# Optimization experiments

Measured on AMD Instinct MI355X. Metric: run time of the kernel, lower is better.

## Reference

```python
import jax, jax.numpy as jnp
import numpy as np

N_NODES = 50000
N_EDGES = 1_600_000
HIDDEN = 128
BOND = 16


def setup_inputs() -> dict:
    key = jax.random.key(0)
    ks = jax.random.split(key, 6)
    h = jax.random.normal(ks[0], (N_NODES, HIDDEN), dtype=jnp.float32)
    edge_index = jax.random.randint(ks[1], (2, N_EDGES), 0, N_NODES, dtype=jnp.int32)
    bond_features = jax.random.normal(ks[2], (N_EDGES, BOND), dtype=jnp.float32)
    fan_in1 = 2 * HIDDEN + BOND
    W1 = jax.random.normal(ks[3], (fan_in1, HIDDEN), dtype=jnp.float32) / np.sqrt(fan_in1)
    b1 = jnp.zeros((HIDDEN,), dtype=jnp.float32)
    W2 = jax.random.normal(ks[4], (HIDDEN, HIDDEN), dtype=jnp.float32) / np.sqrt(HIDDEN)
    b2 = jnp.zeros((HIDDEN,), dtype=jnp.float32)
    return {"h": h, "edge_index": edge_index, "bond_features": bond_features,
            "W1": W1, "b1": b1, "W2": W2, "b2": b2}


def reference(h, edge_index, bond_features, W1, b1, W2, b2):
    row, col = edge_index[0], edge_index[1]
    # gather endpoint features + bond features -> [E, 2H+B]
    msgs = jnp.concatenate([h[row], h[col], bond_features], axis=-1)
    # 2-layer MLP with SiLU
    msgs = jax.nn.silu(msgs @ W1 + b1) @ W2 + b2  # [E, H]
    # scatter-add back to source nodes (index_add_ on row)
    h_out = jax.ops.segment_sum(msgs, row, num_segments=h.shape[0])
    return h_out
```

## Files before the change

kernel.cpp:

```cpp
#include <hip/hip_runtime.h>

typedef __attribute__((ext_vector_type(4))) float  f32x4;
typedef __attribute__((ext_vector_type(2))) float  f32x2;
typedef __attribute__((ext_vector_type(8))) short  s16x8;
typedef __attribute__((ext_vector_type(4))) float  f4v;
typedef __attribute__((ext_vector_type(4))) int    i32x4;

#define MFMA_BF16 __builtin_amdgcn_mfma_f32_16x16x32_bf16
#define SENT 0x7fffffff

#if defined(__has_builtin)
#if __has_builtin(__builtin_amdgcn_cvt_pk_fp8_f32) && __has_builtin(__builtin_amdgcn_cvt_pk_f32_fp8)
#define HW8 1
#endif
#endif

__device__ __forceinline__ short f2bf(float f) {
  unsigned u = __builtin_bit_cast(unsigned, f);
  u += 0x7fffu + ((u >> 16) & 1u);
  return (short)(u >> 16);
}
__device__ __forceinline__ float bf2f(short s) {
  unsigned u = ((unsigned)(unsigned short)s) << 16;
  return __builtin_bit_cast(float, u);
}
__device__ __forceinline__ s16x8 cvt8(f4v f0, f4v f1) {
  s16x8 r;
  r[0] = f2bf(f0[0]); r[1] = f2bf(f0[1]); r[2] = f2bf(f0[2]); r[3] = f2bf(f0[3]);
  r[4] = f2bf(f1[0]); r[5] = f2bf(f1[1]); r[6] = f2bf(f1[2]); r[7] = f2bf(f1[3]);
  return r;
}
__device__ __forceinline__ unsigned cvtpk_bf16(float a, float b) {
  unsigned r;
  asm("v_cvt_pk_bf16_f32 %0, %1, %2" : "=v"(r) : "v"(a), "v"(b));
  return r;
}
__device__ __forceinline__ unsigned f2fp8(float x) {
  unsigned u = __builtin_bit_cast(unsigned, x);
  unsigned s = (u >> 24) & 0x80u;
  unsigned au = u & 0x7fffffffu;
  if (au < 0x3C800000u) return s;
  unsigned biased = au - 0x3C000000u;
  unsigned val = biased >> 20;
  unsigned rem = biased & 0xFFFFFu;
  val += (rem > 0x80000u) || (rem == 0x80000u && (val & 1u));
  if (val > 0x7Eu) val = 0x7Eu;
  return s | val;
}
__device__ __forceinline__ float fp8tof(unsigned b) {
  unsigned em = b & 0x7fu;
  unsigned f = ((em + 960u) << 20) | ((b & 0x80u) << 24);
  return (em < 8u) ? 0.f : __builtin_bit_cast(float, f);
}
__device__ __forceinline__ unsigned char enc_fp8(float x) {
#ifdef HW8
  return (unsigned char)(__builtin_amdgcn_cvt_pk_fp8_f32(x, x, 0u, false) & 0xffu);
#else
  return (unsigned char)f2fp8(x);
#endif
}
__device__ __forceinline__ unsigned enc_fp8x4(f4v v) {
#ifdef HW8
  unsigned u = __builtin_amdgcn_cvt_pk_fp8_f32(v[0], v[1], 0u, false);
  u = __builtin_amdgcn_cvt_pk_fp8_f32(v[2], v[3], u, true);
  return u;
#else
  return f2fp8(v[0]) | (f2fp8(v[1]) << 8) | (f2fp8(v[2]) << 16) | (f2fp8(v[3]) << 24);
#endif
}
__device__ __forceinline__ void dec_fp8x4(unsigned d, float* f) {
#ifdef HW8
  f32x2 lo = __builtin_amdgcn_cvt_pk_f32_fp8(d, false);
  f32x2 hi = __builtin_amdgcn_cvt_pk_f32_fp8(d, true);
  f[0] = lo[0]; f[1] = lo[1]; f[2] = hi[0]; f[3] = hi[1];
#else
#pragma unroll
  for (int j = 0; j < 4; ++j) f[j] = fp8tof((d >> (8 * j)) & 0xffu);
#endif
}

__global__ __launch_bounds__(256) void prep_weights(
    const float* __restrict__ W1, const float* __restrict__ W2,
    short* __restrict__ wp, float* __restrict__ out, int outN4,
    int* __restrict__ cnt, int NN) {
  int t = blockIdx.x * 256 + threadIdx.x;
  int total = gridDim.x * 256;
  if (out) {
    f32x4* o4 = reinterpret_cast<f32x4*>(out);
    for (int i = t; i < outN4; i += total) o4[i] = (f32x4){0.f, 0.f, 0.f, 0.f};
  }
  if (cnt) {
    for (int i = t; i < NN; i += total) cnt[i] = 0;
  }
  int chunk = t >> 6, l = t & 63;
  if (chunk >= 104) return;
  int q = l >> 4, c = l & 15;
  s16x8 v;
  if (chunk < 72) {
    int kk = chunk >> 3, nt = chunk & 7;
    int k0 = kk * 32 + q * 8, n = nt * 16 + c;
#pragma unroll
    for (int j = 0; j < 8; ++j) {
      int k = k0 + j;
      v[j] = (k < 272) ? f2bf(W1[k * 128 + n]) : (short)0;
    }
    *reinterpret_cast<s16x8*>(wp + (size_t)chunk * 512 + l * 8) = v;
  } else {
    int c2 = chunk - 72;
    int kk = c2 >> 3, nt = c2 & 7;
    int k0 = kk * 32 + q * 8, n = nt * 16 + c;
#pragma unroll
    for (int j = 0; j < 8; ++j) v[j] = f2bf(W2[(k0 + j) * 128 + n]);
    *reinterpret_cast<s16x8*>(wp + 36864 + (size_t)c2 * 512 + l * 8) = v;
  }
}

#define NB_H 512
__global__ __launch_bounds__(256) void k_gh(
    const float* __restrict__ h, const short* __restrict__ wp,
    short* __restrict__ Gs, const int* __restrict__ ei,
    int* __restrict__ cnt, int NN, int NB_G, int E) {
  if ((int)blockIdx.x >= NB_G) {
    int i = ((int)blockIdx.x - NB_G) * 256 + threadIdx.x;
    for (; i < E; i += NB_H * 256) atomicAdd(&cnt[ei[i]], 1);
    return;
  }
  const int tid = threadIdx.x;
  const int w = tid >> 6, l = tid & 63;
  const int q = l >> 4, c = l & 15;
  const int nb = blockIdx.x * 64 + w * 16;

  f32x4 acc[16];
#pragma unroll
  for (int nt = 0; nt < 16; ++nt) acc[nt] = (f32x4){0.f, 0.f, 0.f, 0.f};

#pragma unroll
  for (int kk = 0; kk < 4; ++kk) {
    int node = nb + c; if (node >= NN) node = NN - 1;
    const float* src = h + (size_t)node * 128 + kk * 32 + q * 8;
    s16x8 a = cvt8(*reinterpret_cast<const f4v*>(src),
                   *reinterpret_cast<const f4v*>(src + 4));
#pragma unroll
    for (int nt2 = 0; nt2 < 16; ++nt2) {
      int kkg = kk + ((nt2 >= 8) ? 4 : 0);
      int chunk = kkg * 8 + (nt2 & 7);
      s16x8 b = *reinterpret_cast<const s16x8*>(wp + (size_t)chunk * 512 + l * 8);
      acc[nt2] = MFMA_BF16(a, b, acc[nt2], 0, 0, 0);
    }
  }
  unsigned char* Gb = (unsigned char*)Gs;
#pragma unroll
  for (int nt2 = 0; nt2 < 16; ++nt2)
#pragma unroll
    for (int r = 0; r < 4; ++r) {
      int node = nb + q * 4 + r;
      if (node < NN) {
        if (nt2 < 8) {
          Gs[(size_t)node * 192 + nt2 * 16 + c] = f2bf(acc[nt2][r]);
        } else {
          int n7 = nt2 - 8;
          int addr = ((n7 & 1) * 2 + (c >> 3)) * 32 + (n7 >> 1) * 8 + (c & 7);
          Gb[(size_t)node * 384 + 256 + addr] = enc_fp8(acc[nt2][r]);
        }
      }
    }
}

__global__ __launch_bounds__(1024) void k_s1(const int* __restrict__ cnt,
                                             int* __restrict__ partial, int NN) {
  __shared__ int red[16];
  int t = threadIdx.x, idx = blockIdx.x * 1024 + t;
  int v = (idx < NN) ? cnt[idx] : 0;
#pragma unroll
  for (int d = 1; d < 64; d <<= 1) v += __shfl_xor(v, d);
  if ((t & 63) == 0) red[t >> 6] = v;
  __syncthreads();
  if (t == 0) {
    int s = 0;
#pragma unroll
    for (int i = 0; i < 16; ++i) s += red[i];
    partial[blockIdx.x] = s;
  }
}
__global__ __launch_bounds__(1024) void k_s3m(int* __restrict__ cnt,
                                              const int* __restrict__ partial,
                                              int NN) {
  __shared__ int ps[1024];
  __shared__ int pbuf[64];
  __shared__ int base_s;
  int t = threadIdx.x, bid = blockIdx.x, idx = bid * 1024 + t;
  if (t < 64) pbuf[t] = (t < bid) ? partial[t] : 0;
  int v = (idx < NN) ? cnt[idx] : 0;
  ps[t] = v;
  __syncthreads();
  if (t == 0) {
    int b = 0;
#pragma unroll
    for (int j = 0; j < 64; ++j) b += pbuf[j];
    base_s = b;
  }
  for (int d = 1; d < 1024; d <<= 1) {
    int u = (t >= d) ? ps[t - d] : 0;
    __syncthreads(); ps[t] += u; __syncthreads();
  }
  if (idx < NN) cnt[idx] = ps[t] - v + base_s;
}

__global__ void k_scatter13(const int* __restrict__ ei, int* __restrict__ cnt,
                            int* __restrict__ rc, unsigned* __restrict__ bond8,
                            const float* __restrict__ bond, int E) {
  int i = blockIdx.x * blockDim.x + threadIdx.x;
  int stride = gridDim.x * blockDim.x;
  for (; i < E; i += stride) {
    int r = ei[i], c = ei[(size_t)E + i];
    int pos = atomicAdd(&cnt[r], 1);
    rc[pos] = r | (c << 16);
    const f4v* b4 = reinterpret_cast<const f4v*>(bond + (size_t)i * 16);
    i32x4 o;
    o[0] = (int)enc_fp8x4(b4[0]);
    o[1] = (int)enc_fp8x4(b4[1]);
    o[2] = (int)enc_fp8x4(b4[2]);
    o[3] = (int)enc_fp8x4(b4[3]);
    *reinterpret_cast<i32x4*>(bond8 + (size_t)pos * 4) = o;
  }
}

__global__ __launch_bounds__(512, 4) void edge_mlp14(
    const short* __restrict__ Gs, const int* __restrict__ rc,
    const unsigned* __restrict__ bond8, const short* __restrict__ wp,
    const float* __restrict__ b1, const float* __restrict__ b2,
    float* __restrict__ out, int E) {
  __shared__ __align__(16) char ubuf[8 * 16 * 136 * 2];
  __shared__ __align__(16) short wlds[20480];
  short (*Plds)[16][136] = reinterpret_cast<short(*)[16][136]>(ubuf);
  float (*Sred)[16][68]  = reinterpret_cast<float(*)[16][68]>(ubuf);

  const int tid = threadIdx.x;
  const int w = tid >> 6, l = tid & 63;
  const int q = l >> 4, c = l & 15;

  {
    const s16x8* src = reinterpret_cast<const s16x8*>(wp + 32768);
    s16x8* dst = reinterpret_cast<s16x8*>(wlds);
#pragma unroll
    for (int i = 0; i < 5; ++i) dst[tid + i * 512] = src[tid + i * 512];
  }
  __syncthreads();
  const short* wl1 = wlds;
  const short* wl2 = wlds + 4096;

  int nwg = gridDim.x;
  int qq = nwg >> 3, rr = nwg & 7;
  int xcd = blockIdx.x & 7, idx = blockIdx.x >> 3;
  int sbid = (xcd < rr ? xcd * (qq + 1) : rr * (qq + 1) + (xcd - rr) * qq) + idx;
  const int eb = sbid * 128;
  const int we = w * 16;

  int rcv = 0xFFFF;
  if (l < 16) {
    int gpos = eb + we + l;
    if (gpos < E) rcv = rc[gpos];
  }
  int v = __shfl(rcv, c);
  int rv = v & 0xffff;
  int rA = (rv == 0xFFFF) ? 0 : rv;
  int cA = ((unsigned)v) >> 16;

  int vn = __shfl(rcv, (l + 1) & 63);
  unsigned long long bm = __ballot(
      (l < 16) && ((rcv & 0xffff) != ((l < 15) ? (vn & 0xffff) : -1)));

  s16x8 g1v[4];
  i32x4 g2v[2];
  s16x8 az = {};
  {
    const short* gb = Gs + (size_t)rA * 192;
#pragma unroll
    for (int kk = 0; kk < 4; ++kk)
      g1v[kk] = *reinterpret_cast<const s16x8*>(gb + kk * 32 + q * 8);
    const char* g2b = (const char*)Gs + (size_t)cA * 384 + 256 + q * 32;
    g2v[0] = *reinterpret_cast<const i32x4*>(g2b);
    g2v[1] = *reinterpret_cast<const i32x4*>(g2b + 16);
    if (q < 2) {
      int ge = eb + we + c; if (ge >= E) ge = E - 1;
      uint2 d = *reinterpret_cast<const uint2*>(bond8 + (size_t)ge * 4 + q * 2);
      float f[8];
      dec_fp8x4(d.x, f);
      dec_fp8x4(d.y, f + 4);
      i32x4 aw;
#pragma unroll
      for (int p = 0; p < 4; ++p)
        aw[p] = (int)cvtpk_bf16(f[2 * p], f[2 * p + 1]);
      az = __builtin_bit_cast(s16x8, aw);
    }
  }

  f32x4 acc[8];
#pragma unroll
  for (int nt = 0; nt < 8; ++nt) acc[nt] = (f32x4){0.f, 0.f, 0.f, 0.f};
  __builtin_amdgcn_s_setprio(1);
#pragma unroll
  for (int nt = 0; nt < 8; ++nt) {
    s16x8 b = *reinterpret_cast<const s16x8*>(wl1 + nt * 512 + l * 8);
    acc[nt] = MFMA_BF16(az, b, acc[nt], 0, 0, 0);
  }
  __builtin_amdgcn_s_setprio(0);

#pragma unroll
  for (int nt = 0; nt < 8; ++nt) {
    float bias = b1[nt * 16 + c];
    unsigned p01 = cvtpk_bf16(acc[nt][0] + bias, acc[nt][1] + bias);
    unsigned p23 = cvtpk_bf16(acc[nt][2] + bias, acc[nt][3] + bias);
    Plds[w][q * 4 + 0][nt * 16 + c] = (short)(p01 & 0xffffu);
    Plds[w][q * 4 + 1][nt * 16 + c] = (short)(p01 >> 16);
    Plds[w][q * 4 + 2][nt * 16 + c] = (short)(p23 & 0xffffu);
    Plds[w][q * 4 + 3][nt * 16 + c] = (short)(p23 >> 16);
  }

#pragma unroll
  for (int nt = 0; nt < 8; ++nt) acc[nt] = (f32x4){0.f, 0.f, 0.f, 0.f};

#pragma unroll
  for (int kk = 0; kk < 4; ++kk) {
    s16x8 gk = g1v[kk];
    unsigned d0 = (unsigned)g2v[kk >> 1][(kk & 1) * 2 + 0];
    unsigned d1 = (unsigned)g2v[kk >> 1][(kk & 1) * 2 + 1];
    float g2f[8];
    dec_fp8x4(d0, g2f);
    dec_fp8x4(d1, g2f + 4);
    s16x8 pb = *reinterpret_cast<const s16x8*>(&Plds[w][c][kk * 32 + q * 8]);
    float sv[8];
#pragma unroll
    for (int j = 0; j < 8; ++j) {
      float x = bf2f(gk[j]) + g2f[j] + bf2f(pb[j]);
      float e = __expf(-x);
      sv[j] = x * __builtin_amdgcn_rcpf(1.f + e);
    }
    i32x4 a2w;
#pragma unroll
    for (int p = 0; p < 4; ++p)
      a2w[p] = (int)cvtpk_bf16(sv[2 * p], sv[2 * p + 1]);
    s16x8 a2 = __builtin_bit_cast(s16x8, a2w);
    __builtin_amdgcn_s_setprio(1);
#pragma unroll
    for (int nt = 0; nt < 8; ++nt) {
      s16x8 b = *reinterpret_cast<const s16x8*>(wl2 + (kk * 8 + nt) * 512 + l * 8);
      acc[nt] = MFMA_BF16(a2, b, acc[nt], 0, 0, 0);
    }
    __builtin_amdgcn_s_setprio(0);
  }

#pragma unroll
  for (int h2 = 0; h2 < 2; ++h2) {
#pragma unroll
    for (int nt2 = 0; nt2 < 4; ++nt2) {
      int nt = h2 * 4 + nt2;
      float bias = b2[nt * 16 + c];
#pragma unroll
      for (int r = 0; r < 4; ++r)
        Sred[w][q * 4 + r][nt2 * 16 + c] = acc[nt][r] + bias;
    }
    float vsum = 0.f;
#pragma unroll
    for (int r = 0; r < 16; ++r) {
      vsum += Sred[w][r][l];
      if ((bm >> r) & 1ull) {
        int rowv = __shfl(rcv, r) & 0xffff;
        if (rowv != 0xFFFF)
          unsafeAtomicAdd(&out[(size_t)rowv * 128 + h2 * 64 + l], vsum);
        vsum = 0.f;
      }
    }
  }
}

__global__ __launch_bounds__(256, 2) void edge_mlp(
    const float* __restrict__ h, const int* __restrict__ ei,
    const float* __restrict__ bond, const short* __restrict__ wp,
    const float* __restrict__ b1, const float* __restrict__ b2,
    float* __restrict__ out, int E) {
  __shared__ __align__(16) short Plds[4][64][136];
  __shared__ int rows_s[256];
  __shared__ int cols_s[256];
  const int tid = threadIdx.x;
  const int w = tid >> 6, l = tid & 63;
  const int q = l >> 4, c = l & 15;
  const int eb = blockIdx.x * 256;
  {
    int e = eb + tid; if (e >= E) e = E - 1;
    rows_s[tid] = ei[e];
    cols_s[tid] = ei[(size_t)E + e];
  }
  __syncthreads();
  const int we = w * 64;
  int rN[4], cN[4], eI[4];
#pragma unroll
  for (int mi = 0; mi < 4; ++mi) {
    int el = we + mi * 16 + c;
    rN[mi] = rows_s[el]; cN[mi] = cols_s[el];
    int eg = eb + el; if (eg >= E) eg = E - 1;
    eI[mi] = eg;
  }
  f32x4 acc[4][8];
#pragma unroll
  for (int mi = 0; mi < 4; ++mi)
#pragma unroll
    for (int nt = 0; nt < 8; ++nt) acc[mi][nt] = (f32x4){0.f, 0.f, 0.f, 0.f};
#pragma unroll
  for (int part = 0; part < 2; ++part) {
#pragma unroll
    for (int kk = 0; kk < 4; ++kk) {
      s16x8 a[4];
#pragma unroll
      for (int mi = 0; mi < 4; ++mi) {
        int node = part ? cN[mi] : rN[mi];
        const float* src = h + (size_t)node * 128 + kk * 32 + q * 8;
        a[mi] = cvt8(*reinterpret_cast<const f4v*>(src),
                     *reinterpret_cast<const f4v*>(src + 4));
      }
      const int kkg = part * 4 + kk;
#pragma unroll
      for (int nt = 0; nt < 8; ++nt) {
        s16x8 b = *reinterpret_cast<const s16x8*>(wp + (size_t)(kkg * 8 + nt) * 512 + l * 8);
#pragma unroll
        for (int mi = 0; mi < 4; ++mi)
          acc[mi][nt] = MFMA_BF16(a[mi], b, acc[mi][nt], 0, 0, 0);
      }
    }
  }
  {
    s16x8 a[4];
#pragma unroll
    for (int mi = 0; mi < 4; ++mi) {
      s16x8 az = {};
      if (q < 2) {
        const float* src = bond + (size_t)eI[mi] * 16 + q * 8;
        az = cvt8(*reinterpret_cast<const f4v*>(src),
                  *reinterpret_cast<const f4v*>(src + 4));
      }
      a[mi] = az;
    }
#pragma unroll
    for (int nt = 0; nt < 8; ++nt) {
      s16x8 b = *reinterpret_cast<const s16x8*>(wp + (size_t)(64 + nt) * 512 + l * 8);
#pragma unroll
      for (int mi = 0; mi < 4; ++mi)
        acc[mi][nt] = MFMA_BF16(a[mi], b, acc[mi][nt], 0, 0, 0);
    }
  }
#pragma unroll
  for (int nt = 0; nt < 8; ++nt) {
    float bias = b1[nt * 16 + c];
#pragma unroll
    for (int mi = 0; mi < 4; ++mi)
#pragma unroll
      for (int r = 0; r < 4; ++r) {
        float x = acc[mi][nt][r] + bias;
        float s = x / (1.f + __expf(-x));
        Plds[w][mi * 16 + q * 4 + r][nt * 16 + c] = f2bf(s);
      }
  }
  f32x4 acc2[4][8];
#pragma unroll
  for (int mi = 0; mi < 4; ++mi)
#pragma unroll
    for (int nt = 0; nt < 8; ++nt) acc2[mi][nt] = (f32x4){0.f, 0.f, 0.f, 0.f};
#pragma unroll
  for (int kk = 0; kk < 4; ++kk) {
    s16x8 a2[4];
#pragma unroll
    for (int mi = 0; mi < 4; ++mi)
      a2[mi] = *reinterpret_cast<const s16x8*>(&Plds[w][mi * 16 + c][kk * 32 + q * 8]);
#pragma unroll
    for (int nt = 0; nt < 8; ++nt) {
      s16x8 b = *reinterpret_cast<const s16x8*>(wp + 36864 + (size_t)(kk * 8 + nt) * 512 + l * 8);
#pragma unroll
      for (int mi = 0; mi < 4; ++mi)
        acc2[mi][nt] = MFMA_BF16(a2[mi], b, acc2[mi][nt], 0, 0, 0);
    }
  }
#pragma unroll
  for (int nt = 0; nt < 8; ++nt) {
    float bias = b2[nt * 16 + c];
#pragma unroll
    for (int mi = 0; mi < 4; ++mi)
#pragma unroll
      for (int r = 0; r < 4; ++r) {
        int el = we + mi * 16 + q * 4 + r;
        if ((eb + el) < E) {
          int node = rows_s[el];
          unsafeAtomicAdd(&out[(size_t)node * 128 + nt * 16 + c],
                          acc2[mi][nt][r] + bias);
        }
      }
  }
}

extern "C" void kernel_launch(void* const* d_in, const int* in_sizes, int n_in,
                              void* d_out, int out_size, void* d_ws, size_t ws_size,
                              hipStream_t stream) {
  const float* h    = (const float*)d_in[0];
  const int*   ei   = (const int*)d_in[1];
  const float* bond = (const float*)d_in[2];
  const float* W1   = (const float*)d_in[3];
  const float* b1   = (const float*)d_in[4];
  const float* W2   = (const float*)d_in[5];
  const float* b2   = (const float*)d_in[6];
  float* out = (float*)d_out;
  char* ws = (char*)d_ws;

  const int E  = in_sizes[1] / 2;
  const int NN = in_sizes[0] / 128;

  short* wp = (short*)ws;
  size_t off_G    = 131072;
  size_t off_cnt  = off_G + (size_t)NN * 384;
  size_t off_par  = off_cnt + (((size_t)NN * 4 + 15) & ~15ull);
  size_t off_idx  = off_par + 4096;
  size_t off_bs   = off_idx + (((size_t)E * 4 + 15) & ~15ull);
  size_t need14   = off_bs + (size_t)E * 16;

  if (ws_size >= need14 && NN <= 65535) {
    short*    Gs    = (short*)(ws + off_G);
    int*      cnt   = (int*)(ws + off_cnt);
    int*      par   = (int*)(ws + off_par);
    int*      rc    = (int*)(ws + off_idx);
    unsigned* bond8 = (unsigned*)(ws + off_bs);
    const int NB_G = (NN + 63) / 64;
    const int P    = (NN + 1023) / 1024;

    prep_weights<<<512, 256, 0, stream>>>(W1, W2, wp, out, NN * 32, cnt, NN);
    k_gh<<<NB_G + NB_H, 256, 0, stream>>>(h, wp, Gs, ei, cnt, NN, NB_G, E);
    k_s1<<<P, 1024, 0, stream>>>(cnt, par, NN);
    k_s3m<<<P, 1024, 0, stream>>>(cnt, par, NN);
    k_scatter13<<<2048, 256, 0, stream>>>(ei, cnt, rc, bond8, bond, E);
    edge_mlp14<<<(E + 127) / 128, 512, 0, stream>>>(Gs, rc, bond8, wp, b1, b2, out, E);
  } else {
    hipMemsetAsync(d_out, 0, (size_t)NN * 128 * sizeof(float), stream);
    prep_weights<<<512, 256, 0, stream>>>(W1, W2, wp, (float*)nullptr, 0,
                                          (int*)nullptr, 0);
    edge_mlp<<<(E + 255) / 256, 256, 0, stream>>>(h, ei, bond, wp, b1, b2, out, E);
  }
}
```

Measured before the change: 385.0 us.

## Fuse scan, output zeroing and edge scatter into one cooperative kernel

Replaces the separate block-sum, scan and scatter launches with a single cooperative kernel. It uses grid-wide syncs to compute the per-node prefix offsets and then bucket edges with fp8 bond encoding. The output zeroing moves from prep_weights into the idle blocks of the scan phase, and prep_weights drops to 64 blocks. This removes two launch boundaries and takes work off prep_weights, at the cost of grid.sync overhead and a fixed grid of 1024 blocks for the scatter loop. It falls back to the old path if the cooperative launch fails.

Measured after the change: 611.4 us. 1.59x slower.

```diff
diff --git a/kernel.cpp b/kernel.cpp
--- a/kernel.cpp
+++ b/kernel.cpp
@@ -1,4 +1,6 @@
 #include <hip/hip_runtime.h>
+#include <hip/hip_cooperative_groups.h>
+namespace cg = cooperative_groups;
 
 typedef __attribute__((ext_vector_type(4))) float  f32x4;
 typedef __attribute__((ext_vector_type(2))) float  f32x2;
@@ -164,6 +166,59 @@
         }
       }
     }
+}
+
+__global__ __launch_bounds__(256) void k_sss(
+    const int* __restrict__ ei, int* __restrict__ cnt, int* __restrict__ par,
+    int* __restrict__ rc, unsigned* __restrict__ bond8,
+    const float* __restrict__ bond, float* __restrict__ out,
+    int E, int NN, int outN4) {
+  cg::grid_group grid = cg::this_grid();
+  __shared__ int ps[256];
+  __shared__ int red[4];
+  const int t = threadIdx.x, bid = blockIdx.x;
+  const int P = (NN + 255) >> 8;
+  const int idx = bid * 256 + t;
+  int v = 0;
+  if (bid < P) {
+    v = (idx < NN) ? cnt[idx] : 0;
+    ps[t] = v;
+    __syncthreads();
+    for (int d = 1; d < 256; d <<= 1) {
+      int u = (t >= d) ? ps[t - d] : 0;
+      __syncthreads(); ps[t] += u; __syncthreads();
+    }
+    if (t == 255) par[bid] = ps[255];
+  } else {
+    f32x4* o4 = reinterpret_cast<f32x4*>(out);
+    int nb = gridDim.x - P;
+    for (int i = (bid - P) * 256 + t; i < outN4; i += nb * 256)
+      o4[i] = (f32x4){0.f, 0.f, 0.f, 0.f};
+  }
+  grid.sync();
+  if (bid < P) {
+    int pv = (t < bid) ? par[t] : 0;
+#pragma unroll
+    for (int d = 1; d < 64; d <<= 1) pv += __shfl_xor(pv, d);
+    if ((t & 63) == 0) red[t >> 6] = pv;
+    __syncthreads();
+    int base = red[0] + red[1] + red[2] + red[3];
+    if (idx < NN) cnt[idx] = ps[t] - v + base;
+  }
+  grid.sync();
+  const int stride = gridDim.x * 256;
+  for (int i = bid * 256 + t; i < E; i += stride) {
+    int r = ei[i], c = ei[(size_t)E + i];
+    int pos = atomicAdd(&cnt[r], 1);
+    rc[pos] = r | (c << 16);
+    const f4v* b4 = reinterpret_cast<const f4v*>(bond + (size_t)i * 16);
+    i32x4 o;
+    o[0] = (int)enc_fp8x4(b4[0]);
+    o[1] = (int)enc_fp8x4(b4[1]);
+    o[2] = (int)enc_fp8x4(b4[2]);
+    o[3] = (int)enc_fp8x4(b4[3]);
+    *reinterpret_cast<i32x4*>(bond8 + (size_t)pos * 4) = o;
+  }
 }
 
 __global__ __launch_bounds__(1024) void k_s1(const int* __restrict__ cnt,
@@ -205,7 +260,6 @@
   }
   if (idx < NN) cnt[idx] = ps[t] - v + base_s;
 }
-
 __global__ void k_scatter13(const int* __restrict__ ei, int* __restrict__ cnt,
                             int* __restrict__ rc, unsigned* __restrict__ bond8,
                             const float* __restrict__ bond, int E) {
@@ -518,27 +572,39 @@
   size_t off_par  = off_cnt + (((size_t)NN * 4 + 15) & ~15ull);
   size_t off_idx  = off_par + 4096;
   size_t off_bs   = off_idx + (((size_t)E * 4 + 15) & ~15ull);
-  size_t need14   = off_bs + (size_t)E * 16;
-
-  if (ws_size >= need14 && NN <= 65535) {
+  size_t need15   = off_bs + (size_t)E * 16;
+
+  if (ws_size >= need15 && NN <= 65535) {
     short*    Gs    = (short*)(ws + off_G);
     int*      cnt   = (int*)(ws + off_cnt);
     int*      par   = (int*)(ws + off_par);
     int*      rc    = (int*)(ws + off_idx);
     unsigned* bond8 = (unsigned*)(ws + off_bs);
     const int NB_G = (NN + 63) / 64;
-    const int P    = (NN + 1023) / 1024;
-
-    prep_weights<<<512, 256, 0, stream>>>(W1, W2, wp, out, NN * 32, cnt, NN);
+    int outN4 = NN * 32;
+    int E_ = E, NN_ = NN;
+
+    prep_weights<<<64, 256, 0, stream>>>(W1, W2, wp, (float*)nullptr, 0, cnt, NN);
     k_gh<<<NB_G + NB_H, 256, 0, stream>>>(h, wp, Gs, ei, cnt, NN, NB_G, E);
-    k_s1<<<P, 1024, 0, stream>>>(cnt, par, NN);
-    k_s3m<<<P, 1024, 0, stream>>>(cnt, par, NN);
-    k_scatter13<<<2048, 256, 0, stream>>>(ei, cnt, rc, bond8, bond, E);
+
+    void* args[] = {(void*)&ei, (void*)&cnt, (void*)&par, (void*)&rc,
+                    (void*)&bond8, (void*)&bond, (void*)&out,
+                    (void*)&E_, (void*)&NN_, (void*)&outN4};
+    hipError_t ce = hipLaunchCooperativeKernel((const void*)k_sss,
+                                               dim3(1024), dim3(256),
+                                               args, 0, stream);
+    if (ce != hipSuccess) {
+      hipMemsetAsync(out, 0, (size_t)NN * 128 * sizeof(float), stream);
+      const int P = (NN + 1023) / 1024;
+      k_s1<<<P, 1024, 0, stream>>>(cnt, par, NN);
+      k_s3m<<<P, 1024, 0, stream>>>(cnt, par, NN);
+      k_scatter13<<<2048, 256, 0, stream>>>(ei, cnt, rc, bond8, bond, E);
+    }
     edge_mlp14<<<(E + 127) / 128, 512, 0, stream>>>(Gs, rc, bond8, wp, b1, b2, out, E);
   } else {
     hipMemsetAsync(d_out, 0, (size_t)NN * 128 * sizeof(float), stream);
-    prep_weights<<<512, 256, 0, stream>>>(W1, W2, wp, (float*)nullptr, 0,
-                                          (int*)nullptr, 0);
+    prep_weights<<<64, 256, 0, stream>>>(W1, W2, wp, (float*)nullptr, 0,
+                                         (int*)nullptr, 0);
     edge_mlp<<<(E + 255) / 256, 256, 0, stream>>>(h, ei, bond, wp, b1, b2, out, E);
   }
 }
```
